# Optimization experiments

Measured on AMD Instinct MI355X. Metric: run time of the kernel, lower is better.

Reference implementation:

```python
import jax, jax.numpy as jnp
import numpy as np
from jax import lax

B, N, NPOINT = 8, 8192, 1024
NSAMPLE = (16, 32)
IN_CH = 64
MLPS = ((64, 64, 128), (64, 96, 128))
EPS = 1e-5


def setup_inputs() -> dict:
    key = jax.random.key(0)
    ks = jax.random.split(key, 16)
    inp = {}
    inp["xyz"] = jax.random.normal(ks[0], (B, 3, N), jnp.float32)
    inp["points"] = jax.random.normal(ks[1], (B, IN_CH, N), jnp.float32)
    ki = 2
    for i, mlp in enumerate(MLPS):
        last = IN_CH + 3
        for j, out in enumerate(mlp):
            inp["w%d_%d" % (i, j)] = jax.random.normal(ks[ki], (out, last), jnp.float32) * (1.0 / float(np.sqrt(last)))
            inp["b%d_%d" % (i, j)] = jnp.zeros((out,), jnp.float32)
            inp["g%d_%d" % (i, j)] = jnp.ones((out,), jnp.float32)
            inp["be%d_%d" % (i, j)] = jnp.zeros((out,), jnp.float32)
            ki += 1
            last = out
    return inp


def _fps(xyz_t):
    # farthest point sampling; xyz_t: [B, N, 3] -> [B, NPOINT] int32
    Bb, Nn, _ = xyz_t.shape

    def step(carry, _):
        dist, far = carry
        c = jnp.take_along_axis(xyz_t, far[:, None, None], axis=1)  # [B,1,3]
        d = jnp.sum((xyz_t - c) ** 2, -1)
        dist = jnp.minimum(dist, d)
        return (dist, jnp.argmax(dist, -1).astype(jnp.int32)), far

    init = (jnp.full((Bb, Nn), 1e10, jnp.float32), jnp.zeros((Bb,), jnp.int32))
    _, cent = lax.scan(step, init, None, length=NPOINT)
    return cent.T  # [B, NPOINT]


def _gather(p, idx):
    # p: [B, N, C], idx: [B, ...] -> [B, ..., C]
    return jax.vmap(lambda a, i: a[i])(p, idx)


def _sqdist(a, b):
    # a: [B, S, 3], b: [B, N, 3] -> [B, S, N] squared euclidean distance
    return (jnp.sum(a * a, -1)[:, :, None] + jnp.sum(b * b, -1)[:, None, :]
            - 2.0 * jnp.einsum('bsc,bnc->bsn', a, b))


def _mlp(x, params):
    # x: [B, C, S, K]; 1x1 Conv2d + BatchNorm2d (batch stats, training mode) + ReLU
    for w, b, g, be in params:
        x = jnp.einsum('oc,bcsk->bosk', w, x) + b[None, :, None, None]
        m = x.mean((0, 2, 3), keepdims=True)
        v = x.var((0, 2, 3), keepdims=True)
        x = (x - m) * lax.rsqrt(v + EPS) * g[None, :, None, None] + be[None, :, None, None]
        x = jax.nn.relu(x)
    return x


def _forward(xyz, points, params):
    xyz_t = jnp.transpose(xyz, (0, 2, 1))     # [B, N, 3]
    pts_t = jnp.transpose(points, (0, 2, 1))  # [B, N, C]
    fps_idx = _fps(xyz_t)
    new_xyz = _gather(xyz_t, fps_idx)         # [B, S, 3]
    outs = []
    for i, k in enumerate(NSAMPLE):
        d = _sqdist(new_xyz, xyz_t)           # [B, S, N]
        _, idx = lax.top_k(-d, k)             # k nearest neighbors
        g_xyz = _gather(xyz_t, idx) - new_xyz[:, :, None, :]  # [B, S, k, 3]
        g_pts = _gather(pts_t, idx)                           # [B, S, k, C]
        feat = jnp.transpose(jnp.concatenate([g_xyz, g_pts], -1), (0, 3, 1, 2))  # [B, 3+C, S, k]
        outs.append(jnp.max(_mlp(feat, params[i]), -1))       # [B, C_out, S]
    return jnp.transpose(new_xyz, (0, 2, 1)), jnp.concatenate(outs, 1)


def reference(xyz, points, w0_0, b0_0, g0_0, be0_0, w0_1, b0_1, g0_1, be0_1, w0_2, b0_2, g0_2, be0_2, w1_0, b1_0, g1_0, be1_0, w1_1, b1_1, g1_1, be1_1, w1_2, b1_2, g1_2, be1_2):
    params = [[(w0_0, b0_0, g0_0, be0_0), (w0_1, b0_1, g0_1, be0_1), (w0_2, b0_2, g0_2, be0_2)],
              [(w1_0, b1_0, g1_0, be1_0), (w1_1, b1_1, g1_1, be1_1), (w1_2, b1_2, g1_2, be1_2)]]
    return _forward(xyz, points, params)
```

## Files before the change

### kernel.cpp

```cpp
#include <hip/hip_runtime.h>
#include <math.h>

#define BN_EPS 1e-5f
constexpr int Bc = 8, Nc = 8192, Sc = 1024, CINc = 64;

typedef float v2f __attribute__((ext_vector_type(2)));
typedef short short8v __attribute__((ext_vector_type(8)));
typedef float f32x4 __attribute__((ext_vector_type(4)));

__device__ __forceinline__ unsigned short f2bf(float f) {
  unsigned u = __float_as_uint(f);
  u += 0x7FFFu + ((u >> 16) & 1u);
  return (unsigned short)(u >> 16);
}
__device__ __forceinline__ float bf2f(unsigned short h) {
  return __uint_as_float(((unsigned)h) << 16);
}

template <int CTRL, int RMASK>
__device__ __forceinline__ unsigned long long dpp_maxu64(unsigned long long k) {
  int lo = (int)(unsigned)k, hi = (int)(unsigned)(k >> 32);
  int olo = __builtin_amdgcn_update_dpp(lo, lo, CTRL, RMASK, 0xF, false);
  int ohi = __builtin_amdgcn_update_dpp(hi, hi, CTRL, RMASK, 0xF, false);
  unsigned long long ok = ((unsigned long long)(unsigned)ohi << 32) | (unsigned)olo;
  return ok > k ? ok : k;
}
template <int CTRL, int RMASK>
__device__ __forceinline__ v2f dpp_sumstep2(v2f v) {
  int olo = __builtin_amdgcn_update_dpp(0, __float_as_int(v.x), CTRL, RMASK, 0xF, false);
  int ohi = __builtin_amdgcn_update_dpp(0, __float_as_int(v.y), CTRL, RMASK, 0xF, false);
  v2f o = {__int_as_float(olo), __int_as_float(ohi)};
  return v + o;
}
__device__ __forceinline__ v2f dpp_sum64v2(v2f v) {
  v = dpp_sumstep2<0x111, 0xF>(v);
  v = dpp_sumstep2<0x112, 0xF>(v);
  v = dpp_sumstep2<0x114, 0xF>(v);
  v = dpp_sumstep2<0x118, 0xF>(v);
  v = dpp_sumstep2<0x142, 0xA>(v);
  v = dpp_sumstep2<0x143, 0xC>(v);
  return v;
}

__device__ __forceinline__ void pproj_body(int i, const float* __restrict__ pts,
                                           const float* __restrict__ wl,
                                           const float* __restrict__ bl,
                                           float* __restrict__ P) {
  int b = i >> 13, n = i & 8191;
  const float* pb = pts + (size_t)b * CINc * Nc + n;
  v2f acc[32];
  const v2f* bl2 = (const v2f*)bl;
#pragma unroll
  for (int o2 = 0; o2 < 32; o2++) acc[o2] = bl2[o2];
  for (int c = 0; c < CINc; c++) {
    float xv = pb[(size_t)c * Nc];
    v2f xv2 = {xv, xv};
    const v2f* wr = (const v2f*)(wl + c * 64);
#pragma unroll
    for (int o2 = 0; o2 < 32; o2++) acc[o2] = __builtin_elementwise_fma(wr[o2], xv2, acc[o2]);
  }
  float4* Pn = (float4*)(P + (size_t)i * 64);
#pragma unroll
  for (int o4 = 0; o4 < 16; o4++)
    Pn[o4] = make_float4(acc[2 * o4].x, acc[2 * o4].y, acc[2 * o4 + 1].x, acc[2 * o4 + 1].y);
}

__global__ __launch_bounds__(512) void mega_kernel(const float* __restrict__ xyz,
                                                   const float* __restrict__ pts,
                                                   const float* __restrict__ w00,
                                                   const float* __restrict__ b00,
                                                   const float* __restrict__ w10,
                                                   const float* __restrict__ b10,
                                                   float4* __restrict__ xyzT,
                                                   float4* __restrict__ nx,
                                                   float* __restrict__ out0,
                                                   float* __restrict__ P0,
                                                   float* __restrict__ P1) {
  __shared__ alignas(16) char smemc[102528];
  int bid = blockIdx.x, t = threadIdx.x;
  if (bid < 8) {
    float* xs = (float*)smemc;
    float* ys = xs + Nc;
    float* zs = ys + Nc;
    int* idxs = (int*)(smemc + 98304);
    unsigned long long* red = (unsigned long long*)(smemc + 102400);
    const float* xb = xyz + (size_t)bid * 3 * Nc;
    float px[16], py[16], pz[16], dd[16];
#pragma unroll
    for (int j = 0; j < 16; j++) {
      int n = j * 512 + t;
      float x = xb[n], y = xb[Nc + n], z = xb[2 * Nc + n];
      px[j] = x; py[j] = y; pz[j] = z;
      xs[n] = x; ys[n] = y; zs[n] = z;
      dd[j] = 1e10f;
    }
    int w = t >> 6;
    __syncthreads();
    int curIdx = 0;
    for (int i = 0; i < Sc; i++) {
      float cx = xs[curIdx], cy = ys[curIdx], cz = zs[curIdx];
      if (t == 0) idxs[i] = curIdx;
      float bd = -1.f;
      int bnidx = 0;
#pragma unroll
      for (int j = 0; j < 16; j++) {
        float dx = px[j] - cx, dy = py[j] - cy, dz = pz[j] - cz;
        float d = fmaf(dz, dz, fmaf(dy, dy, dx * dx));
        d = fminf(dd[j], d);
        dd[j] = d;
        if (d > bd) { bd = d; bnidx = j * 512 + t; }
      }
      unsigned long long key =
          ((unsigned long long)__float_as_uint(bd) << 32) | (unsigned)(~bnidx);
      key = dpp_maxu64<0x111, 0xF>(key);
      key = dpp_maxu64<0x112, 0xF>(key);
      key = dpp_maxu64<0x114, 0xF>(key);
      key = dpp_maxu64<0x118, 0xF>(key);
      key = dpp_maxu64<0x142, 0xA>(key);
      key = dpp_maxu64<0x143, 0xC>(key);
      if ((t & 63) == 63) red[(i & 1) * 8 + w] = key;
      __syncthreads();
      const unsigned long long* rr = red + (i & 1) * 8;
      unsigned long long k2 = rr[0];
#pragma unroll
      for (int u = 1; u < 8; u++) {
        unsigned long long o = rr[u];
        k2 = (o > k2) ? o : k2;
      }
      curIdx = (int)(~(unsigned)(k2 & 0xFFFFFFFFull));
    }
    __syncthreads();
    for (int i2 = t; i2 < Sc; i2 += 512) {
      int idx = idxs[i2];
      float x = xs[idx], y = ys[idx], z = zs[idx];
      nx[bid * Sc + i2] = make_float4(x, y, z, fmaf(z, z, fmaf(y, y, x * x)));
      float* ob = out0 + (size_t)bid * 3 * Sc;
      ob[i2] = x; ob[Sc + i2] = y; ob[2 * Sc + i2] = z;
    }
  } else if (bid < 136) {
    int i = (bid - 8) * 512 + t;
    int b = i >> 13, n = i & 8191;
    const float* xb = xyz + (size_t)b * 3 * Nc;
    float x = xb[n], y = xb[Nc + n], z = xb[2 * Nc + n];
    xyzT[i] = make_float4(x, y, z, fmaf(z, z, fmaf(y, y, x * x)));
  } else {
    bool second = bid >= 264;
    const float* ww = second ? w10 : w00;
    const float* bb = second ? b10 : b00;
    float* PP = second ? P1 : P0;
    float* wl = (float*)smemc;
    float* bl = wl + 64 * 64;
    for (int i2 = t; i2 < 64 * 64; i2 += 512) {
      int c = i2 >> 6, o = i2 & 63;
      wl[i2] = ww[o * 67 + 3 + c];
    }
    if (t < 64) bl[t] = bb[t];
    __syncthreads();
    pproj_body(((bid - (second ? 264 : 136)) * 512) + t, pts, wl, bl, PP);
  }
}

__global__ __launch_bounds__(256) void knn_kernel(const float4* __restrict__ xyzT,
                                                  const float4* __restrict__ newxyz,
                                                  int* __restrict__ knn) {
  int lane = threadIdx.x & 63;
  int sub = lane >> 5;
  int l32 = lane & 31;
  int waveId = blockIdx.x * 4 + (threadIdx.x >> 6);
  int q = waveId * 2 + sub;
  int b = q >> 10;
  float4 qv = newxyz[q];
  const float4* pb = xyzT + (size_t)b * Nc;
  unsigned long long lk = ~0ull;
  unsigned long long worst = ~0ull;
  for (int t0 = 0; t0 < Nc; t0 += 32) {
    float4 p = pb[t0 + l32];
    float dot = fmaf(qv.z, p.z, fmaf(qv.y, p.y, qv.x * p.x));
    float d = fmaf(-2.f, dot, qv.w + p.w);
    unsigned fu = __float_as_uint(d);
    fu ^= (unsigned)(-(int)(fu >> 31)) | 0x80000000u;
    unsigned long long ck = ((unsigned long long)fu << 32) | (unsigned)(t0 + l32);
    unsigned long long bal = __ballot(ck < worst);
    unsigned mymask = (unsigned)(bal >> (sub * 32));
    while (mymask) {
      int src = __ffs(mymask) - 1;
      unsigned long long ckb = __shfl(ck, src, 32);
      unsigned long long bel = __ballot(lk < ckb);
      int cnt = __popc((unsigned)(bel >> (sub * 32)));
      unsigned long long up = __shfl_up(lk, 1, 32);
      lk = (l32 == cnt) ? ckb : ((l32 > cnt) ? up : lk);
      worst = __shfl(lk, 31, 32);
      mymask &= ~(1u << src);
      unsigned long long bal2 = __ballot(ck < worst);
      mymask &= (unsigned)(bal2 >> (sub * 32));
    }
  }
  knn[(size_t)q * 32 + l32] = (int)(lk & 0xFFFFFFFFu);
}

template <int K>
__device__ __forceinline__ void conv1_body(char* smemc, int bidl,
                                           const float4* __restrict__ xyzT,
                                           const float4* __restrict__ nx,
                                           const int* __restrict__ knn,
                                           const float* __restrict__ P,
                                           const float* __restrict__ w0,
                                           unsigned short* __restrict__ y,
                                           float* __restrict__ part, int Pos) {
  v2f* wst = (v2f*)smemc;
  float* wx = (float*)(smemc + 8192);
  float* wy = wx + 64;
  float* wz = wy + 64;
  if (threadIdx.x < 64) {
    int o = threadIdx.x;
    wx[o] = w0[o * 67];
    wy[o] = w0[o * 67 + 1];
    wz[o] = w0[o * 67 + 2];
  }
  __syncthreads();
  int gp = bidl * 256 + threadIdx.x;
  int b = gp / Pos, r = gp % Pos;
  int s = r / K, kk = r & (K - 1);
  int n = knn[((size_t)(b * Sc + s)) * 32 + kk];
  float4 c4 = nx[b * Sc + s];
  float4 p4 = xyzT[(size_t)b * Nc + n];
  v2f dx2 = {p4.x - c4.x, p4.x - c4.x};
  v2f dy2 = {p4.y - c4.y, p4.y - c4.y};
  v2f dz2 = {p4.z - c4.z, p4.z - c4.z};
  const float4* Pn = (const float4*)(P + ((size_t)b * Nc + n) * 64);
  v2f acc[32];
#pragma unroll
  for (int o4 = 0; o4 < 16; o4++) {
    float4 v = Pn[o4];
    acc[2 * o4] = (v2f){v.x, v.y};
    acc[2 * o4 + 1] = (v2f){v.z, v.w};
  }
  const v2f* wx2 = (const v2f*)wx;
  const v2f* wy2 = (const v2f*)wy;
  const v2f* wz2 = (const v2f*)wz;
#pragma unroll
  for (int o2 = 0; o2 < 32; o2++) acc[o2] = __builtin_elementwise_fma(wx2[o2], dx2, acc[o2]);
#pragma unroll
  for (int o2 = 0; o2 < 32; o2++) acc[o2] = __builtin_elementwise_fma(wy2[o2], dy2, acc[o2]);
#pragma unroll
  for (int o2 = 0; o2 < 32; o2++) acc[o2] = __builtin_elementwise_fma(wz2[o2], dz2, acc[o2]);
  unsigned short* yt = y + (size_t)bidl * 64 * 256 + threadIdx.x;
#pragma unroll
  for (int o2 = 0; o2 < 32; o2++) {
    yt[(size_t)(2 * o2) * 256] = f2bf(acc[o2].x);
    yt[(size_t)(2 * o2 + 1) * 256] = f2bf(acc[o2].y);
  }
  int lane = threadIdx.x & 63, w = threadIdx.x >> 6;
  int row = w * 4 + (lane >> 4);
  bool lead = (lane & 15) == 15;
#pragma unroll
  for (int o2 = 0; o2 < 32; o2++) {
    float v0 = acc[o2].x, v1 = acc[o2].y;
    v2f s0 = (v2f){v0, v0 * v0};
    s0 = dpp_sumstep2<0x111, 0xF>(s0);
    s0 = dpp_sumstep2<0x112, 0xF>(s0);
    s0 = dpp_sumstep2<0x114, 0xF>(s0);
    s0 = dpp_sumstep2<0x118, 0xF>(s0);
    v2f s1 = (v2f){v1, v1 * v1};
    s1 = dpp_sumstep2<0x111, 0xF>(s1);
    s1 = dpp_sumstep2<0x112, 0xF>(s1);
    s1 = dpp_sumstep2<0x114, 0xF>(s1);
    s1 = dpp_sumstep2<0x118, 0xF>(s1);
    if (lead) { wst[row * 64 + 2 * o2] = s0; wst[row * 64 + 2 * o2 + 1] = s1; }
  }
  __syncthreads();
  if (threadIdx.x < 64) {
    int o = threadIdx.x;
    v2f sv = (v2f){0.f, 0.f};
#pragma unroll
    for (int rr = 0; rr < 16; rr++) sv += wst[rr * 64 + o];
    ((v2f*)part)[(size_t)bidl * 64 + o] = sv;
  }
}

__global__ __launch_bounds__(256) void conv1M_kernel(
    const float4* xyzT, const float4* nx, const int* knn,
    const float* P0, const float* w0a, unsigned short* y0a, float* part0, int Pos0,
    const float* P1, const float* w0b, unsigned short* y0b, float* part1, int Pos1, int split) {
  __shared__ alignas(16) char smemc[8960];
  if ((int)blockIdx.x < split)
    conv1_body<16>(smemc, blockIdx.x, xyzT, nx, knn, P0, w0a, y0a, part0, Pos0);
  else
    conv1_body<32>(smemc, blockIdx.x - split, xyzT, nx, knn, P1, w0b, y0b, part1, Pos1);
}

__global__ __launch_bounds__(256) void bnfinM_kernel(
    const float* part0, const float* g0, const float* be0, float* bn0, int C0, int nblk0, float inv0,
    const float* part1, const float* g1, const float* be1, float* bn1, int C1, int nblk1, float inv1,
    int split) {
  const float* part; const float* g; const float* be; float* bn;
  int C, nblk, c; float invcnt;
  if ((int)blockIdx.x < split) {
    part = part0; g = g0; be = be0; bn = bn0; C = C0; nblk = nblk0; invcnt = inv0; c = blockIdx.x;
  } else {
    part = part1; g = g1; be = be1; bn = bn1; C = C1; nblk = nblk1; invcnt = inv1; c = blockIdx.x - split;
  }
  v2f sq = (v2f){0.f, 0.f};
  for (int i = threadIdx.x; i < nblk; i += 256) sq += ((const v2f*)part)[(size_t)i * C + c];
  sq = dpp_sum64v2(sq);
  __shared__ v2f ls[4];
  int w = threadIdx.x >> 6;
  if ((threadIdx.x & 63) == 63) ls[w] = sq;
  __syncthreads();
  if (threadIdx.x == 0) {
    v2f tt = ls[0] + ls[1] + ls[2] + ls[3];
    float m = tt.x * invcnt;
    float v = tt.y * invcnt - m * m;
    float sc = g[c] / sqrtf(v + BN_EPS);
    bn[c * 2] = sc;
    bn[c * 2 + 1] = fmaf(-m, sc, be[c]);
  }
}

template <int CI, int CO>
__device__ __forceinline__ void convB_body(char* smemc, int bidl,
                                           const unsigned short* __restrict__ yin,
                                           const float* __restrict__ wt,
                                           const float* __restrict__ bb,
                                           const float* __restrict__ bn,
                                           unsigned short* __restrict__ yout,
                                           float* __restrict__ part, int Pos) {
  constexpr int COq = CO / 4;
  constexpr int COq2 = COq / 2;
  float* wl = (float*)smemc;
  float* bnl = wl + CI * CO;
  float* bl = bnl + 2 * CI;
  for (int i = threadIdx.x; i < CI * CO; i += 256) {
    int c = i / CO, o = i % CO;
    wl[i] = wt[o * CI + c];
  }
  for (int i = threadIdx.x; i < 2 * CI; i += 256) bnl[i] = bn[i];
  if (threadIdx.x < CO) bl[threadIdx.x] = bb[threadIdx.x];
  __syncthreads();
  int w = threadIdx.x >> 6, l = threadIdx.x & 63;
  int cb = w * COq;
  const ushort4* xt = (const ushort4*)(yin + (size_t)bidl * CI * 256) + l;
  v2f acc[4][COq2];
#pragma unroll
  for (int p = 0; p < 4; p++)
#pragma unroll
    for (int q = 0; q < COq2; q++) acc[p][q] = ((const v2f*)(bl + cb))[q];
  ushort4 cur = xt[0], nxt;
  for (int c = 0; c < CI; c++) {
    if (c + 1 < CI) nxt = xt[(c + 1) * 64];
    float scv = bnl[2 * c], shv = bnl[2 * c + 1];
    float xv0 = fmaxf(fmaf(bf2f(cur.x), scv, shv), 0.f);
    float xv1 = fmaxf(fmaf(bf2f(cur.y), scv, shv), 0.f);
    float xv2 = fmaxf(fmaf(bf2f(cur.z), scv, shv), 0.f);
    float xv3 = fmaxf(fmaf(bf2f(cur.w), scv, shv), 0.f);
    v2f x0 = {xv0, xv0}, x1 = {xv1, xv1}, x2 = {xv2, xv2}, x3 = {xv3, xv3};
    const float4* wr = (const float4*)(wl + c * CO + cb);
#pragma unroll
    for (int o4 = 0; o4 < COq / 4; o4++) {
      float4 wv = wr[o4];
      v2f w01 = {wv.x, wv.y}, w23 = {wv.z, wv.w};
      acc[0][2 * o4] = __builtin_elementwise_fma(w01, x0, acc[0][2 * o4]);
      acc[0][2 * o4 + 1] = __builtin_elementwise_fma(w23, x0, acc[0][2 * o4 + 1]);
      acc[1][2 * o4] = __builtin_elementwise_fma(w01, x1, acc[1][2 * o4]);
      acc[1][2 * o4 + 1] = __builtin_elementwise_fma(w23, x1, acc[1][2 * o4 + 1]);
      acc[2][2 * o4] = __builtin_elementwise_fma(w01, x2, acc[2][2 * o4]);
      acc[2][2 * o4 + 1] = __builtin_elementwise_fma(w23, x2, acc[2][2 * o4 + 1]);
      acc[3][2 * o4] = __builtin_elementwise_fma(w01, x3, acc[3][2 * o4]);
      acc[3][2 * o4 + 1] = __builtin_elementwise_fma(w23, x3, acc[3][2 * o4 + 1]);
    }
    cur = nxt;
  }
  unsigned short* yo = yout + (size_t)bidl * CO * 256;
#pragma unroll
  for (int q = 0; q < COq2; q++) {
    ushort4 a, bq;
    a.x = f2bf(acc[0][q].x); a.y = f2bf(acc[1][q].x);
    a.z = f2bf(acc[2][q].x); a.w = f2bf(acc[3][q].x);
    bq.x = f2bf(acc[0][q].y); bq.y = f2bf(acc[1][q].y);
    bq.z = f2bf(acc[2][q].y); bq.w = f2bf(acc[3][q].y);
    ((ushort4*)(yo + (size_t)(cb + 2 * q) * 256))[l] = a;
    ((ushort4*)(yo + (size_t)(cb + 2 * q + 1) * 256))[l] = bq;
  }
#pragma unroll
  for (int q = 0; q < COq2; q++) {
    v2f sv = acc[0][q] + acc[1][q] + acc[2][q] + acc[3][q];
    v2f sq = acc[0][q] * acc[0][q];
    sq = __builtin_elementwise_fma(acc[1][q], acc[1][q], sq);
    sq = __builtin_elementwise_fma(acc[2][q], acc[2][q], sq);
    sq = __builtin_elementwise_fma(acc[3][q], acc[3][q], sq);
    sv = dpp_sum64v2(sv);
    sq = dpp_sum64v2(sq);
    if (l == 63) {
      ((v2f*)part)[(size_t)bidl * CO + cb + 2 * q] = (v2f){sv.x, sq.x};
      ((v2f*)part)[(size_t)bidl * CO + cb + 2 * q + 1] = (v2f){sv.y, sq.y};
    }
  }
}

__global__ __launch_bounds__(256) void conv2M_kernel(
    const unsigned short* y0a, const float* w1a, const float* b1a, const float* bn1a,
    unsigned short* y1a, float* part0, int Pos0,
    const unsigned short* y0b, const float* w1b, const float* b1b, const float* bn1b,
    unsigned short* y1b, float* part1, int Pos1, int split) {
  __shared__ alignas(16) char smemc[25472];
  if ((int)blockIdx.x < split)
    convB_body<64, 64>(smemc, blockIdx.x, y0a, w1a, b1a, bn1a, y1a, part0, Pos0);
  else
    convB_body<64, 96>(smemc, blockIdx.x - split, y0b, w1b, b1b, bn1b, y1b, part1, Pos1);
}

template <int CI, int K>
__device__ __forceinline__ void conv3_mfma_body(char* dsm, int bidl,
                                                const unsigned short* __restrict__ yin,
                                                const float* __restrict__ wt,
                                                const float* __restrict__ bb,
                                                const float* __restrict__ bn,
                                                float* __restrict__ ymax,
                                                float* __restrict__ ymin,
                                                float* __restrict__ part, int Pos) {
  constexpr int CO = 128;
  constexpr int LD = CI + 8;
  unsigned short* Wbf = (unsigned short*)dsm;
  unsigned short* Xbf = Wbf + CO * LD;
  int tid = threadIdx.x;
  for (int i = tid; i < CO * CI; i += 256) {
    int o = i / CI, c = i - o * CI;
    Wbf[o * LD + c] = f2bf(wt[i]);
  }
  const unsigned short* yt = yin + (size_t)bidl * CI * 256;
  for (int i = tid; i < CI * 256; i += 256) {
    int c = i >> 8, p = i & 255;
    float scv = bn[2 * c], shv = bn[2 * c + 1];
    float v = fmaxf(fmaf(bf2f(yt[i]), scv, shv), 0.f);
    Xbf[p * LD + c] = f2bf(v);
  }
  __syncthreads();
  int w = tid >> 6, l = tid & 63;
  int lrow = l & 15, lk = (l >> 4) * 8;
  f32x4 acc[4][8];
#pragma unroll
  for (int Mt = 0; Mt < 4; Mt++)
#pragma unroll
    for (int Nt = 0; Nt < 8; Nt++) acc[Mt][Nt] = (f32x4){0.f, 0.f, 0.f, 0.f};
#pragma unroll
  for (int kt = 0; kt < CI / 32; kt++) {
    short8v a[4], bfr[8];
#pragma unroll
    for (int Mt = 0; Mt < 4; Mt++)
      a[Mt] = *(const short8v*)(Xbf + (w * 64 + Mt * 16 + lrow) * LD + kt * 32 + lk);
#pragma unroll
    for (int Nt = 0; Nt < 8; Nt++)
      bfr[Nt] = *(const short8v*)(Wbf + (Nt * 16 + lrow) * LD + kt * 32 + lk);
#pragma unroll
    for (int Mt = 0; Mt < 4; Mt++)
#pragma unroll
      for (int Nt = 0; Nt < 8; Nt++)
        acc[Mt][Nt] = __builtin_amdgcn_mfma_f32_16x16x32_bf16(a[Mt], bfr[Nt], acc[Mt][Nt], 0, 0, 0);
  }
  __syncthreads();
  float* wstat = (float*)Xbf;
  int bpb = Pos / 256;
  int b = bidl / bpb;
  int posbase = (bidl % bpb) * 256;
#pragma unroll
  for (int Nt = 0; Nt < 8; Nt++) {
    float bv = bb[Nt * 16 + lrow];
    float sv = 0.f, sq = 0.f;
    float mxs[4], mns[4];
#pragma unroll
    for (int Mt = 0; Mt < 4; Mt++) {
      f32x4 a4 = acc[Mt][Nt];
      float v0 = a4.x + bv, v1 = a4.y + bv, v2 = a4.z + bv, v3 = a4.w + bv;
      sv += (v0 + v1) + (v2 + v3);
      sq = fmaf(v0, v0, sq); sq = fmaf(v1, v1, sq);
      sq = fmaf(v2, v2, sq); sq = fmaf(v3, v3, sq);
      mxs[Mt] = fmaxf(fmaxf(v0, v1), fmaxf(v2, v3));
      mns[Mt] = fminf(fminf(v0, v1), fminf(v2, v3));
    }
    if (K == 16) {
#pragma unroll
      for (int Mt = 0; Mt < 4; Mt++) {
        float mx = mxs[Mt], mn = mns[Mt];
        mx = fmaxf(mx, __shfl_xor(mx, 16)); mx = fmaxf(mx, __shfl_xor(mx, 32));
        mn = fminf(mn, __shfl_xor(mn, 16)); mn = fminf(mn, __shfl_xor(mn, 32));
        if (l < 16) {
          int s = (posbase + w * 64 + Mt * 16) >> 4;
          ymax[((size_t)b * CO + Nt * 16 + l) * Sc + s] = mx;
          ymin[((size_t)b * CO + Nt * 16 + l) * Sc + s] = mn;
        }
      }
    } else {
#pragma unroll
      for (int pr = 0; pr < 2; pr++) {
        float mx = fmaxf(mxs[2 * pr], mxs[2 * pr + 1]);
        float mn = fminf(mns[2 * pr], mns[2 * pr + 1]);
        mx = fmaxf(mx, __shfl_xor(mx, 16)); mx = fmaxf(mx, __shfl_xor(mx, 32));
        mn = fminf(mn, __shfl_xor(mn, 16)); mn = fminf(mn, __shfl_xor(mn, 32));
        if (l < 16) {
          int s = (posbase + w * 64 + pr * 32) >> 5;
          ymax[((size_t)b * CO + Nt * 16 + l) * Sc + s] = mx;
          ymin[((size_t)b * CO + Nt * 16 + l) * Sc + s] = mn;
        }
      }
    }
    sv += __shfl_xor(sv, 16); sv += __shfl_xor(sv, 32);
    sq += __shfl_xor(sq, 16); sq += __shfl_xor(sq, 32);
    if (l < 16) {
      wstat[(w * CO + Nt * 16 + l) * 2] = sv;
      wstat[(w * CO + Nt * 16 + l) * 2 + 1] = sq;
    }
  }
  __syncthreads();
  if (tid < CO) {
    v2f tt = (v2f){0.f, 0.f};
#pragma unroll
    for (int ww = 0; ww < 4; ww++) {
      tt.x += wstat[(ww * CO + tid) * 2];
      tt.y += wstat[(ww * CO + tid) * 2 + 1];
    }
    ((v2f*)part)[(size_t)bidl * CO + tid] = tt;
  }
}

__global__ __launch_bounds__(256, 1) void conv3M_kernel(
    const unsigned short* y1a, const float* w2a, const float* b2a, const float* bn2a,
    float* ymax0, float* ymin0, float* part0, int Pos0,
    const unsigned short* y1b, const float* w2b, const float* b2b, const float* bn2b,
    float* ymax1, float* ymin1, float* part1, int Pos1, int split) {
  extern __shared__ __align__(16) char dsm[];
  if ((int)blockIdx.x < split)
    conv3_mfma_body<64, 16>(dsm, blockIdx.x, y1a, w2a, b2a, bn2a, ymax0, ymin0, part0, Pos0);
  else
    conv3_mfma_body<96, 32>(dsm, blockIdx.x - split, y1b, w2b, b2b, bn2b, ymax1, ymin1, part1, Pos1);
}

__global__ __launch_bounds__(256) void bnfin3fM_kernel(
    const float* part0, const float* g0, const float* be0, const float* ymax0,
    const float* ymin0, int nblk0, float inv0, int coff0,
    const float* part1, const float* g1, const float* be1, const float* ymax1,
    const float* ymin1, int nblk1, float inv1, int coff1,
    float* out1, int split) {
  constexpr int C = 128;
  const float* part; const float* g; const float* be; const float* ymaxp; const float* yminp;
  int nblk, c, coff; float invcnt;
  if ((int)blockIdx.x < split) {
    part = part0; g = g0; be = be0; ymaxp = ymax0; yminp = ymin0;
    nblk = nblk0; invcnt = inv0; coff = coff0; c = blockIdx.x;
  } else {
    part = part1; g = g1; be = be1; ymaxp = ymax1; yminp = ymin1;
    nblk = nblk1; invcnt = inv1; coff = coff1; c = blockIdx.x - split;
  }
  v2f sq = (v2f){0.f, 0.f};
  for (int i = threadIdx.x; i < nblk; i += 256) sq += ((const v2f*)part)[(size_t)i * C + c];
  sq = dpp_sum64v2(sq);
  __shared__ v2f ls[4];
  __shared__ float bnc[2];
  int w = threadIdx.x >> 6;
  if ((threadIdx.x & 63) == 63) ls[w] = sq;
  __syncthreads();
  if (threadIdx.x == 0) {
    v2f tt = ls[0] + ls[1] + ls[2] + ls[3];
    float m = tt.x * invcnt;
    float v = tt.y * invcnt - m * m;
    float sc = g[c] / sqrtf(v + BN_EPS);
    bnc[0] = sc;
    bnc[1] = fmaf(-m, sc, be[c]);
  }
  __syncthreads();
  float sc = bnc[0], sh = bnc[1];
  const float* src = (sc >= 0.f) ? ymaxp : yminp;
#pragma unroll
  for (int k = 0; k < 32; k++) {
    int i = k * 256 + threadIdx.x;
    int b = i >> 10, s = i & 1023;
    float v = src[((size_t)b * C + c) * Sc + s];
    out1[((size_t)b * 256 + coff + c) * Sc + s] = fmaxf(fmaf(v, sc, sh), 0.f);
  }
}

extern "C" void kernel_launch(void* const* d_in, const int* in_sizes, int n_in,
                              void* d_out, int out_size, void* d_ws, size_t ws_size,
                              hipStream_t stream) {
  const float* xyz = (const float*)d_in[0];
  const float* pts = (const float*)d_in[1];
  float* ws = (float*)d_ws;
  float* out0 = (float*)d_out;
  float* out1 = out0 + Bc * 3 * Sc;

  float4* xyzT = (float4*)(ws + 0);
  float4* nx = (float4*)(ws + 262144);
  int* knnp = (int*)(ws + 294912);
  float* P0 = ws + 557056;

  const float* d2 = (const float*)d_in[2];
  const float* d3 = (const float*)d_in[3];
  const float* d4 = (const float*)d_in[4];
  const float* d5 = (const float*)d_in[5];
  const float* d6 = (const float*)d_in[6];
  const float* d7 = (const float*)d_in[7];
  const float* d8 = (const float*)d_in[8];
  const float* d9 = (const float*)d_in[9];
  const float* d10 = (const float*)d_in[10];
  const float* d11 = (const float*)d_in[11];
  const float* d12 = (const float*)d_in[12];
  const float* d13 = (const float*)d_in[13];
  const float* d14 = (const float*)d_in[14];
  const float* d15 = (const float*)d_in[15];
  const float* d16 = (const float*)d_in[16];
  const float* d17 = (const float*)d_in[17];
  const float* d18 = (const float*)d_in[18];
  const float* d19 = (const float*)d_in[19];
  const float* d20 = (const float*)d_in[20];
  const float* d21 = (const float*)d_in[21];
  const float* d22 = (const float*)d_in[22];
  const float* d23 = (const float*)d_in[23];
  const float* d24 = (const float*)d_in[24];
  const float* d25 = (const float*)d_in[25];

  float inv0 = 1.f / (float)(Bc * 16384);
  float inv1 = 1.f / (float)(Bc * 32768);
  const int DSM3 = 79872;

  bool merged = ws_size >= (size_t)72254464 * 4;
  if (merged) {
    float* P1 = ws + 4751360;
    unsigned short* y00 = (unsigned short*)(ws + 8945664);
    unsigned short* y01 = (unsigned short*)(ws + 17334272);
    unsigned short* y10 = (unsigned short*)(ws + 34111488);
    unsigned short* y11 = (unsigned short*)(ws + 42500096);
    float* ymax0 = ws + 67665920;
    float* ymin0 = ws + 68714496;
    float* ymax1 = ws + 69763072;
    float* ymin1 = ws + 70811648;
    float* part0 = ws + 71860224;
    float* part1 = ws + 71991296;
    float* bns = ws + 72253440;
    float* bn10 = bns, *bn11 = bns + 256, *bn20 = bns + 512, *bn21 = bns + 768;

    mega_kernel<<<392, 512, 0, stream>>>(xyz, pts, d2, d3, d14, d15, xyzT, nx, out0, P0, P1);
    knn_kernel<<<1024, 256, 0, stream>>>(xyzT, nx, knnp);
    conv1M_kernel<<<1536, 256, 0, stream>>>(xyzT, nx, knnp, P0, d2, y00, part0, 16384, P1, d14,
                                            y01, part1, 32768, 512);
    bnfinM_kernel<<<128, 256, 0, stream>>>(part0, d4, d5, bn10, 64, 512, inv0, part1, d16, d17,
                                           bn11, 64, 1024, inv1, 64);
    conv2M_kernel<<<1536, 256, 0, stream>>>(y00, d6, d7, bn10, y10, part0, 16384, y01, d18, d19,
                                            bn11, y11, part1, 32768, 512);
    bnfinM_kernel<<<160, 256, 0, stream>>>(part0, d8, d9, bn20, 64, 512, inv0, part1, d20, d21,
                                           bn21, 96, 1024, inv1, 64);
    conv3M_kernel<<<1536, 256, DSM3, stream>>>(y10, d10, d11, bn20, ymax0, ymin0, part0, 16384,
                                               y11, d22, d23, bn21, ymax1, ymin1, part1, 32768,
                                               512);
    bnfin3fM_kernel<<<256, 256, 0, stream>>>(part0, d12, d13, ymax0, ymin0, 512, inv0, 0, part1,
                                             d24, d25, ymax1, ymin1, 1024, inv1, 128, out1, 128);
  } else {
    unsigned short* y0 = (unsigned short*)(ws + 4751360);
    unsigned short* y1 = (unsigned short*)(ws + 21528576);
    float* P1 = ws + 29917184;
    float* ymax = ws + 46694400;
    float* ymin = ws + 47742976;
    float* part = ws + 48791552;
    float* bn1 = ws + 49053696;
    float* bn2 = ws + 49053824;

    mega_kernel<<<392, 512, 0, stream>>>(xyz, pts, d2, d3, d14, d15, xyzT, nx, out0, P0, P1);
    knn_kernel<<<1024, 256, 0, stream>>>(xyzT, nx, knnp);

    conv1M_kernel<<<512, 256, 0, stream>>>(xyzT, nx, knnp, P0, d2, y0, part, 16384, P0, d2, y0,
                                           part, 16384, 512);
    bnfinM_kernel<<<64, 256, 0, stream>>>(part, d4, d5, bn1, 64, 512, inv0, part, d4, d5, bn1, 64,
                                          512, inv0, 64);
    conv2M_kernel<<<512, 256, 0, stream>>>(y0, d6, d7, bn1, y1, part, 16384, y0, d6, d7, bn1, y1,
                                           part, 16384, 512);
    bnfinM_kernel<<<64, 256, 0, stream>>>(part, d8, d9, bn2, 64, 512, inv0, part, d8, d9, bn2, 64,
                                          512, inv0, 64);
    conv3M_kernel<<<512, 256, DSM3, stream>>>(y1, d10, d11, bn2, ymax, ymin, part, 16384, y1, d10,
                                              d11, bn2, ymax, ymin, part, 16384, 512);
    bnfin3fM_kernel<<<128, 256, 0, stream>>>(part, d12, d13, ymax, ymin, 512, inv0, 0, part, d12,
                                             d13, ymax, ymin, 512, inv0, 0, out1, 128);

    conv1M_kernel<<<1024, 256, 0, stream>>>(xyzT, nx, knnp, P1, d14, y0, part, 32768, P1, d14, y0,
                                            part, 32768, 0);
    bnfinM_kernel<<<64, 256, 0, stream>>>(part, d16, d17, bn1, 64, 1024, inv1, part, d16, d17,
                                          bn1, 64, 1024, inv1, 0);
    conv2M_kernel<<<1024, 256, 0, stream>>>(y0, d18, d19, bn1, y1, part, 32768, y0, d18, d19, bn1,
                                            y1, part, 32768, 0);
    bnfinM_kernel<<<96, 256, 0, stream>>>(part, d20, d21, bn2, 96, 1024, inv1, part, d20, d21,
                                          bn2, 96, 1024, inv1, 0);
    conv3M_kernel<<<1024, 256, DSM3, stream>>>(y1, d22, d23, bn2, ymax, ymin, part, 32768, y1,
                                               d22, d23, bn2, ymax, ymin, part, 32768, 0);
    bnfin3fM_kernel<<<128, 256, 0, stream>>>(part, d24, d25, ymax, ymin, 1024, inv1, 128, part,
                                             d24, d25, ymax, ymin, 1024, inv1, 128, out1, 0);
  }
  (void)in_sizes; (void)n_in; (void)out_size; (void)ws_size;
}
```

Baseline: 1.243 ms.

## Rewrite second MLP conv layer with bf16 MFMA and LDS-staged output

Replaces the scalar packed-FMA second 1x1 conv with a bf16 MFMA 16x16x32 implementation. Weights and BN+ReLU-normalized inputs are staged into padded LDS in bf16. Outputs are transposed through LDS for coalesced stores, and per-channel sum/sumsq partials are reduced across waves in shared memory. This adds bf16 rounding of the weights and activations before the matmul and uses about 64KB of dynamic LDS, which with launch_bounds(256,1) may lower occupancy.

```diff
diff --git a/kernel.cpp b/kernel.cpp
--- a/kernel.cpp
+++ b/kernel.cpp
@@ -7,6 +7,7 @@
 typedef float v2f __attribute__((ext_vector_type(2)));
 typedef short short8v __attribute__((ext_vector_type(8)));
 typedef float f32x4 __attribute__((ext_vector_type(4)));
+typedef unsigned short u16x8 __attribute__((ext_vector_type(8)));
 
 __device__ __forceinline__ unsigned short f2bf(float f) {
   unsigned u = __float_as_uint(f);
@@ -318,95 +319,104 @@
 }
 
 template <int CI, int CO>
-__device__ __forceinline__ void convB_body(char* smemc, int bidl,
-                                           const unsigned short* __restrict__ yin,
-                                           const float* __restrict__ wt,
-                                           const float* __restrict__ bb,
-                                           const float* __restrict__ bn,
-                                           unsigned short* __restrict__ yout,
-                                           float* __restrict__ part, int Pos) {
-  constexpr int COq = CO / 4;
-  constexpr int COq2 = COq / 2;
-  float* wl = (float*)smemc;
-  float* bnl = wl + CI * CO;
-  float* bl = bnl + 2 * CI;
-  for (int i = threadIdx.x; i < CI * CO; i += 256) {
-    int c = i / CO, o = i % CO;
-    wl[i] = wt[o * CI + c];
-  }
-  for (int i = threadIdx.x; i < 2 * CI; i += 256) bnl[i] = bn[i];
-  if (threadIdx.x < CO) bl[threadIdx.x] = bb[threadIdx.x];
-  __syncthreads();
-  int w = threadIdx.x >> 6, l = threadIdx.x & 63;
-  int cb = w * COq;
-  const ushort4* xt = (const ushort4*)(yin + (size_t)bidl * CI * 256) + l;
-  v2f acc[4][COq2];
-#pragma unroll
-  for (int p = 0; p < 4; p++)
-#pragma unroll
-    for (int q = 0; q < COq2; q++) acc[p][q] = ((const v2f*)(bl + cb))[q];
-  ushort4 cur = xt[0], nxt;
-  for (int c = 0; c < CI; c++) {
-    if (c + 1 < CI) nxt = xt[(c + 1) * 64];
-    float scv = bnl[2 * c], shv = bnl[2 * c + 1];
-    float xv0 = fmaxf(fmaf(bf2f(cur.x), scv, shv), 0.f);
-    float xv1 = fmaxf(fmaf(bf2f(cur.y), scv, shv), 0.f);
-    float xv2 = fmaxf(fmaf(bf2f(cur.z), scv, shv), 0.f);
-    float xv3 = fmaxf(fmaf(bf2f(cur.w), scv, shv), 0.f);
-    v2f x0 = {xv0, xv0}, x1 = {xv1, xv1}, x2 = {xv2, xv2}, x3 = {xv3, xv3};
-    const float4* wr = (const float4*)(wl + c * CO + cb);
-#pragma unroll
-    for (int o4 = 0; o4 < COq / 4; o4++) {
-      float4 wv = wr[o4];
-      v2f w01 = {wv.x, wv.y}, w23 = {wv.z, wv.w};
-      acc[0][2 * o4] = __builtin_elementwise_fma(w01, x0, acc[0][2 * o4]);
-      acc[0][2 * o4 + 1] = __builtin_elementwise_fma(w23, x0, acc[0][2 * o4 + 1]);
-      acc[1][2 * o4] = __builtin_elementwise_fma(w01, x1, acc[1][2 * o4]);
-      acc[1][2 * o4 + 1] = __builtin_elementwise_fma(w23, x1, acc[1][2 * o4 + 1]);
-      acc[2][2 * o4] = __builtin_elementwise_fma(w01, x2, acc[2][2 * o4]);
-      acc[2][2 * o4 + 1] = __builtin_elementwise_fma(w23, x2, acc[2][2 * o4 + 1]);
-      acc[3][2 * o4] = __builtin_elementwise_fma(w01, x3, acc[3][2 * o4]);
-      acc[3][2 * o4 + 1] = __builtin_elementwise_fma(w23, x3, acc[3][2 * o4 + 1]);
-    }
-    cur = nxt;
-  }
+__device__ __forceinline__ void conv2_mfma_body(char* dsm, int bidl,
+                                                const unsigned short* __restrict__ yin,
+                                                const float* __restrict__ wt,
+                                                const float* __restrict__ bb,
+                                                const float* __restrict__ bn,
+                                                unsigned short* __restrict__ yout,
+                                                float* __restrict__ part) {
+  constexpr int LD = CI + 8;
+  constexpr int NT = CO / 16;
+  constexpr int LDO = 272;
+  unsigned short* Wbf = (unsigned short*)dsm;
+  unsigned short* Xbf = Wbf + CO * LD;
+  int tid = threadIdx.x;
+  for (int i = tid; i < CO * CI; i += 256) {
+    int o = i / CI, c = i - o * CI;
+    Wbf[o * LD + c] = f2bf(wt[i]);
+  }
+  const unsigned short* yt = yin + (size_t)bidl * CI * 256;
+  for (int i = tid; i < CI * 256; i += 256) {
+    int c = i >> 8, p = i & 255;
+    float v = fmaxf(fmaf(bf2f(yt[i]), bn[2 * c], bn[2 * c + 1]), 0.f);
+    Xbf[p * LD + c] = f2bf(v);
+  }
+  __syncthreads();
+  int w = tid >> 6, l = tid & 63;
+  int lrow = l & 15, lk = (l >> 4) * 8;
+  f32x4 acc[4][NT];
+#pragma unroll
+  for (int Mt = 0; Mt < 4; Mt++)
+#pragma unroll
+    for (int Nt = 0; Nt < NT; Nt++) acc[Mt][Nt] = (f32x4){0.f, 0.f, 0.f, 0.f};
+#pragma unroll
+  for (int kt = 0; kt < CI / 32; kt++) {
+    short8v a[4], bfr[NT];
+#pragma unroll
+    for (int Mt = 0; Mt < 4; Mt++)
+      a[Mt] = *(const short8v*)(Xbf + (w * 64 + Mt * 16 + lrow) * LD + kt * 32 + lk);
+#pragma unroll
+    for (int Nt = 0; Nt < NT; Nt++)
+      bfr[Nt] = *(const short8v*)(Wbf + (Nt * 16 + lrow) * LD + kt * 32 + lk);
+#pragma unroll
+    for (int Mt = 0; Mt < 4; Mt++)
+#pragma unroll
+      for (int Nt = 0; Nt < NT; Nt++)
+        acc[Mt][Nt] = __builtin_amdgcn_mfma_f32_16x16x32_bf16(a[Mt], bfr[Nt], acc[Mt][Nt], 0, 0, 0);
+  }
+  __syncthreads();
+  unsigned short* Obuf = (unsigned short*)dsm;
+  float* wstat = (float*)(dsm + CO * LDO * 2);
+#pragma unroll
+  for (int Nt = 0; Nt < NT; Nt++) {
+    float bv = bb[Nt * 16 + lrow];
+    float sv = 0.f, sq = 0.f;
+#pragma unroll
+    for (int Mt = 0; Mt < 4; Mt++) {
+      f32x4 a4 = acc[Mt][Nt];
+      float v0 = a4.x + bv, v1 = a4.y + bv, v2 = a4.z + bv, v3 = a4.w + bv;
+      sv += (v0 + v1) + (v2 + v3);
+      sq = fmaf(v0, v0, sq); sq = fmaf(v1, v1, sq);
+      sq = fmaf(v2, v2, sq); sq = fmaf(v3, v3, sq);
+      ushort4 pk;
+      pk.x = f2bf(v0); pk.y = f2bf(v1); pk.z = f2bf(v2); pk.w = f2bf(v3);
+      *(ushort4*)(Obuf + (Nt * 16 + lrow) * LDO + w * 64 + Mt * 16 + (l >> 4) * 4) = pk;
+    }
+    sv += __shfl_xor(sv, 16); sv += __shfl_xor(sv, 32);
+    sq += __shfl_xor(sq, 16); sq += __shfl_xor(sq, 32);
+    if (l < 16) {
+      wstat[(w * CO + Nt * 16 + l) * 2] = sv;
+      wstat[(w * CO + Nt * 16 + l) * 2 + 1] = sq;
+    }
+  }
+  __syncthreads();
   unsigned short* yo = yout + (size_t)bidl * CO * 256;
-#pragma unroll
-  for (int q = 0; q < COq2; q++) {
-    ushort4 a, bq;
-    a.x = f2bf(acc[0][q].x); a.y = f2bf(acc[1][q].x);
-    a.z = f2bf(acc[2][q].x); a.w = f2bf(acc[3][q].x);
-    bq.x = f2bf(acc[0][q].y); bq.y = f2bf(acc[1][q].y);
-    bq.z = f2bf(acc[2][q].y); bq.w = f2bf(acc[3][q].y);
-    ((ushort4*)(yo + (size_t)(cb + 2 * q) * 256))[l] = a;
-    ((ushort4*)(yo + (size_t)(cb + 2 * q + 1) * 256))[l] = bq;
-  }
-#pragma unroll
-  for (int q = 0; q < COq2; q++) {
-    v2f sv = acc[0][q] + acc[1][q] + acc[2][q] + acc[3][q];
-    v2f sq = acc[0][q] * acc[0][q];
-    sq = __builtin_elementwise_fma(acc[1][q], acc[1][q], sq);
-    sq = __builtin_elementwise_fma(acc[2][q], acc[2][q], sq);
-    sq = __builtin_elementwise_fma(acc[3][q], acc[3][q], sq);
-    sv = dpp_sum64v2(sv);
-    sq = dpp_sum64v2(sq);
-    if (l == 63) {
-      ((v2f*)part)[(size_t)bidl * CO + cb + 2 * q] = (v2f){sv.x, sq.x};
-      ((v2f*)part)[(size_t)bidl * CO + cb + 2 * q + 1] = (v2f){sv.y, sq.y};
-    }
-  }
-}
-
-__global__ __launch_bounds__(256) void conv2M_kernel(
+  for (int i = tid; i < CO * 32; i += 256) {
+    int co = i >> 5, seg = i & 31;
+    *(u16x8*)(yo + co * 256 + seg * 8) = *(const u16x8*)(Obuf + co * LDO + seg * 8);
+  }
+  if (tid < CO) {
+    v2f tt = (v2f){0.f, 0.f};
+#pragma unroll
+    for (int ww = 0; ww < 4; ww++) {
+      tt.x += wstat[(ww * CO + tid) * 2];
+      tt.y += wstat[(ww * CO + tid) * 2 + 1];
+    }
+    ((v2f*)part)[(size_t)bidl * CO + tid] = tt;
+  }
+}
+
+__global__ __launch_bounds__(256, 1) void conv2M_kernel(
     const unsigned short* y0a, const float* w1a, const float* b1a, const float* bn1a,
     unsigned short* y1a, float* part0, int Pos0,
     const unsigned short* y0b, const float* w1b, const float* b1b, const float* bn1b,
     unsigned short* y1b, float* part1, int Pos1, int split) {
-  __shared__ alignas(16) char smemc[25472];
+  extern __shared__ __align__(16) char dsm2[];
   if ((int)blockIdx.x < split)
-    convB_body<64, 64>(smemc, blockIdx.x, y0a, w1a, b1a, bn1a, y1a, part0, Pos0);
+    conv2_mfma_body<64, 64>(dsm2, blockIdx.x, y0a, w1a, b1a, bn1a, y1a, part0);
   else
-    convB_body<64, 96>(smemc, blockIdx.x - split, y0b, w1b, b1b, bn1b, y1b, part1, Pos1);
+    conv2_mfma_body<64, 96>(dsm2, blockIdx.x - split, y0b, w1b, b1b, bn1b, y1b, part1);
 }
 
 template <int CI, int K>
@@ -620,6 +630,7 @@
   float inv0 = 1.f / (float)(Bc * 16384);
   float inv1 = 1.f / (float)(Bc * 32768);
   const int DSM3 = 79872;
+  const int DSM2 = 64512;
 
   bool merged = ws_size >= (size_t)72254464 * 4;
   if (merged) {
@@ -643,8 +654,8 @@
                                             y01, part1, 32768, 512);
     bnfinM_kernel<<<128, 256, 0, stream>>>(part0, d4, d5, bn10, 64, 512, inv0, part1, d16, d17,
                                            bn11, 64, 1024, inv1, 64);
-    conv2M_kernel<<<1536, 256, 0, stream>>>(y00, d6, d7, bn10, y10, part0, 16384, y01, d18, d19,
-                                            bn11, y11, part1, 32768, 512);
+    conv2M_kernel<<<1536, 256, DSM2, stream>>>(y00, d6, d7, bn10, y10, part0, 16384, y01, d18,
+                                               d19, bn11, y11, part1, 32768, 512);
     bnfinM_kernel<<<160, 256, 0, stream>>>(part0, d8, d9, bn20, 64, 512, inv0, part1, d20, d21,
                                            bn21, 96, 1024, inv1, 64);
     conv3M_kernel<<<1536, 256, DSM3, stream>>>(y10, d10, d11, bn20, ymax0, ymin0, part0, 16384,
@@ -669,8 +680,8 @@
                                            part, 16384, 512);
     bnfinM_kernel<<<64, 256, 0, stream>>>(part, d4, d5, bn1, 64, 512, inv0, part, d4, d5, bn1, 64,
                                           512, inv0, 64);
-    conv2M_kernel<<<512, 256, 0, stream>>>(y0, d6, d7, bn1, y1, part, 16384, y0, d6, d7, bn1, y1,
-                                           part, 16384, 512);
+    conv2M_kernel<<<512, 256, DSM2, stream>>>(y0, d6, d7, bn1, y1, part, 16384, y0, d6, d7, bn1,
+                                              y1, part, 16384, 512);
     bnfinM_kernel<<<64, 256, 0, stream>>>(part, d8, d9, bn2, 64, 512, inv0, part, d8, d9, bn2, 64,
                                           512, inv0, 64);
     conv3M_kernel<<<512, 256, DSM3, stream>>>(y1, d10, d11, bn2, ymax, ymin, part, 16384, y1, d10,
@@ -682,8 +693,8 @@
                                             part, 32768, 0);
     bnfinM_kernel<<<64, 256, 0, stream>>>(part, d16, d17, bn1, 64, 1024, inv1, part, d16, d17,
                                           bn1, 64, 1024, inv1, 0);
-    conv2M_kernel<<<1024, 256, 0, stream>>>(y0, d18, d19, bn1, y1, part, 32768, y0, d18, d19, bn1,
-                                            y1, part, 32768, 0);
+    conv2M_kernel<<<1024, 256, DSM2, stream>>>(y0, d18, d19, bn1, y1, part, 32768, y0, d18, d19,
+                                               bn1, y1, part, 32768, 0);
     bnfinM_kernel<<<96, 256, 0, stream>>>(part, d20, d21, bn2, 96, 1024, inv1, part, d20, d21,
                                           bn2, 96, 1024, inv1, 0);
     conv3M_kernel<<<1024, 256, DSM3, stream>>>(y1, d22, d23, bn2, ymax, ymin, part, 32768, y1,
```

After: 1.192 ms. 1.04x faster.
